# Kernel optimization log

Hardware: AMD Instinct MI355X
Metric: run time of the kernel (lower is better)

Reference implementation:

```python
import jax, jax.numpy as jnp
import numpy as np

N_NODES = 100000
N_EDGES = 2000000


def _mlp3(h, w1, b1, w2, b2, w3, b3):
    h = jax.nn.relu(h @ w1.T + b1)
    h = jax.nn.relu(h @ w2.T + b2)
    return h @ w3.T + b3


def setup_inputs() -> dict:
    key = jax.random.key(0)
    ks = jax.random.split(key, 24)
    inp = {
        "x": jax.random.normal(ks[0], (N_NODES, 3), dtype=jnp.float32),
        "edge_index": jax.random.randint(ks[1], (2, N_EDGES), 0, N_NODES, dtype=jnp.int64),
        "edge_attr": jax.random.normal(ks[2], (N_EDGES, 4), dtype=jnp.float32),
    }
    # MLP params (PyTorch Linear: y = x @ W.T + b)
    shapes = {
        "r1_w1": (40, 10), "r1_b1": (40,), "r1_w2": (40, 40), "r1_b2": (40,), "r1_w3": (4, 40), "r1_b3": (4,),
        "o_w1": (40, 7), "o_b1": (40,), "o_w2": (40, 40), "o_b2": (40,), "o_w3": (3, 40), "o_b3": (3,),
        "r2_w1": (40, 10), "r2_b1": (40,), "r2_w2": (40, 40), "r2_b2": (40,), "r2_w3": (1, 40), "r2_b3": (1,),
    }
    for i, (name, shp) in enumerate(shapes.items()):
        inp[name] = jax.random.normal(ks[3 + i], shp, dtype=jnp.float32) * 0.1
    return inp


def reference(x, edge_index, edge_attr,
              r1_w1, r1_b1, r1_w2, r1_b2, r1_w3, r1_b3,
              o_w1, o_b1, o_w2, o_b2, o_w3, o_b3,
              r2_w1, r2_b1, r2_w2, r2_b2, r2_w3, r2_b3):
    n = x.shape[0]
    src, dst = edge_index[0], edge_index[1]  # x_j <- src, x_i <- dst
    # message: relational MLP R1 over [x_i, x_j, edge_attr]  -> [E,4]
    m1 = jnp.concatenate([x[dst], x[src], edge_attr], axis=1)
    e_msg = _mlp3(m1, r1_w1, r1_b1, r1_w2, r1_b2, r1_w3, r1_b3)
    # aggregate: scatter-add messages to destination nodes -> [N,4]
    aggr = jax.ops.segment_sum(e_msg, dst, num_segments=n)
    # update: object MLP O over [x, aggr] -> [N,3]
    x_tilde = _mlp3(jnp.concatenate([x, aggr], axis=1), o_w1, o_b1, o_w2, o_b2, o_w3, o_b3)
    # edge classifier R2 over [x_tilde_i, x_tilde_j, E] -> sigmoid [E,1]
    m2 = jnp.concatenate([x_tilde[dst], x_tilde[src], e_msg], axis=1)
    return jax.nn.sigmoid(_mlp3(m2, r2_w1, r2_b1, r2_w2, r2_b2, r2_w3, r2_b3))
```

## Files before the change

kernel.cpp:

```cpp
#include <hip/hip_runtime.h>
#include <math.h>


typedef __fp16 hf8 __attribute__((ext_vector_type(8)));
typedef _Float16 f16x2 __attribute__((ext_vector_type(2)));
typedef float f32x16 __attribute__((ext_vector_type(16)));
typedef unsigned u32x4 __attribute__((ext_vector_type(4)));

#define NEPC  64
#define BS    4096
#define NBMAX 32
#define TS    1024
#define NFRAG 11

__device__ __forceinline__ f32x16 mfma16(hf8 a, hf8 b, f32x16 c) {
    return __builtin_amdgcn_mfma_f32_32x32x16_f16(a, b, c, 0, 0, 0);
}
__device__ __forceinline__ unsigned pk2(float a, float b) {
    return __builtin_bit_cast(unsigned, __builtin_amdgcn_cvt_pkrtz(a, b));
}
__device__ __forceinline__ unsigned pk2_relu(float a, float b) {
    return __builtin_bit_cast(unsigned,
        __builtin_amdgcn_cvt_pkrtz(fmaxf(a, 0.f), fmaxf(b, 0.f)));
}
__device__ __forceinline__ unsigned pswap(unsigned v) {
    return (unsigned)__shfl_xor((int)v, 32, 64);
}
__device__ __forceinline__ hf8 frag_from(unsigned a, unsigned b, unsigned c, unsigned d) {
    u32x4 v = {a, b, c, d};
    return __builtin_bit_cast(hf8, v);
}

__device__ __forceinline__ void build_frags(const f32x16& t0, const f32x16& t1,
                                            int hi, hf8& F0, hf8& F1, hf8& F2) {
    const unsigned w0 = pk2_relu(t0[0],  t0[1]);
    const unsigned w1 = pk2_relu(t0[2],  t0[3]);
    const unsigned w2 = pk2_relu(t0[4],  t0[5]);
    const unsigned w3 = pk2_relu(t0[6],  t0[7]);
    const unsigned w4 = pk2_relu(t0[8],  t0[9]);
    const unsigned w5 = pk2_relu(t0[10], t0[11]);
    const unsigned w6 = pk2_relu(t0[12], t0[13]);
    const unsigned w7 = pk2_relu(t0[14], t0[15]);
    const unsigned w8 = pk2_relu(t1[0],  t1[1]);
    const unsigned w9 = pk2_relu(t1[2],  t1[3]);
    const unsigned p0 = pswap(w0), p1 = pswap(w1), p2 = pswap(w2), p3 = pswap(w3);
    const unsigned p4 = pswap(w4), p5 = pswap(w5), p6 = pswap(w6), p7 = pswap(w7);
    const unsigned p8 = pswap(w8), p9 = pswap(w9);
    F0 = frag_from(hi ? p2 : w0, hi ? p3 : w1, hi ? w2 : p0, hi ? w3 : p1);
    F1 = frag_from(hi ? p6 : w4, hi ? p7 : w5, hi ? w6 : p4, hi ? w7 : p5);
    F2 = frag_from(hi ? 0x00003c00u : w8, hi ? 0u : w9, hi ? 0u : p8, hi ? 0u : p9);
}

template<int IN, int OUT>
__device__ hf8 load_wfrag(const float* __restrict__ w, const float* __restrict__ b,
                          int mt, int ks, int lane) {
    const int r = mt * 32 + (lane & 31);
    const int kbase = ks * 16 + ((lane >> 5) & 1) * 8;
    hf8 f;
#pragma unroll
    for (int j = 0; j < 8; ++j) {
        const int k = kbase + j;
        float v = 0.f;
        if (r < OUT) {
            if (k < IN) v = w[r * IN + k];
            else if (k == IN) v = b[r];
        }
        f[j] = (__fp16)v;
    }
    return f;
}

template<int OUT>
__device__ hf8 load_wfrag_l1(const float* __restrict__ w, const float* __restrict__ b,
                             int mt, int lane) {
    const int r = mt * 32 + (lane & 31);
    const int kbase = ((lane >> 5) & 1) * 8;
    hf8 f;
#pragma unroll
    for (int j = 0; j < 8; ++j) {
        const int k = kbase + j;
        float v = 0.f;
        if (r < OUT) {
            int src = -1;
            if (k < 3) src = k;
            else if (k >= 4 && k < 7) src = k - 1;
            else if (k >= 8 && k < 12) src = k - 2;
            if (src >= 0) v = w[r * 10 + src];
            else if (k == 12) v = b[r];
        }
        f[j] = (__fp16)v;
    }
    return f;
}

template<int OUT3>
__global__ __launch_bounds__(64) void wprep_kernel(
    const float* __restrict__ w1, const float* __restrict__ b1,
    const float* __restrict__ w2, const float* __restrict__ b2,
    const float* __restrict__ w3, const float* __restrict__ b3,
    uint4* __restrict__ tab)
{
    const int lane = threadIdx.x;
#pragma unroll
    for (int t = 0; t < 2; ++t)
        tab[t * 64 + lane] = __builtin_bit_cast(uint4, load_wfrag_l1<40>(w1, b1, t, lane));
#pragma unroll
    for (int t = 0; t < 2; ++t)
#pragma unroll
        for (int s = 0; s < 3; ++s)
            tab[(2 + t * 3 + s) * 64 + lane] =
                __builtin_bit_cast(uint4, load_wfrag<40, 40>(w2, b2, t, s, lane));
#pragma unroll
    for (int s = 0; s < 3; ++s)
        tab[(8 + s) * 64 + lane] =
            __builtin_bit_cast(uint4, load_wfrag<40, OUT3>(w3, b3, 0, s, lane));
}

template<bool IS_MSG>
__global__ __launch_bounds__(256, 2) void edge_kernel(
    const uint2* __restrict__ nodef,
    const int*   __restrict__ ei,
    const void*  __restrict__ eattr,
    const uint4* __restrict__ wtab,
    uint2* __restrict__ emsg_out,
    float* __restrict__ out,
    int n_edges)
{
    const int lane = threadIdx.x & 63;
    const int ecol = lane & 31;
    const int hi = lane >> 5;

    hf8 wa1[2], wa2[2][3], wa3[3];
    wa1[0] = __builtin_bit_cast(hf8, wtab[0 * 64 + lane]);
    wa1[1] = __builtin_bit_cast(hf8, wtab[1 * 64 + lane]);
#pragma unroll
    for (int t = 0; t < 2; ++t)
#pragma unroll
        for (int s = 0; s < 3; ++s)
            wa2[t][s] = __builtin_bit_cast(hf8, wtab[(2 + t * 3 + s) * 64 + lane]);
#pragma unroll
    for (int s = 0; s < 3; ++s)
        wa3[s] = __builtin_bit_cast(hf8, wtab[(8 + s) * 64 + lane]);

    const int gwave = (int)((blockIdx.x * blockDim.x + threadIdx.x) >> 6);
    const int nwave = (int)((gridDim.x * blockDim.x) >> 6);
    const int nchunk = (n_edges + NEPC - 1) / NEPC;
    const int last = n_edges - 1;

    int c = gwave;
    if (c >= nchunk) return;
    auto eclampX = [&](int cc) { int e = cc * NEPC + ecol;      return e < last ? e : last; };
    auto eclampY = [&](int cc) { int e = cc * NEPC + 32 + ecol; return e < last ? e : last; };

    uint2 fAX, fBX, fAY, fBY;
    int sNX = 0, dNX = 0, sNY = 0, dNY = 0;
    {
        const int eX = eclampX(c), eY = eclampY(c);
        if (hi == 0) {
            const int sX = ei[eX], dX = ei[n_edges + eX];
            const int sY = ei[eY], dY = ei[n_edges + eY];
            fAX = nodef[dX]; fBX = nodef[sX];
            fAY = nodef[dY]; fBY = nodef[sY];
            const int e2X = eclampX(c + nwave), e2Y = eclampY(c + nwave);
            sNX = ei[e2X]; dNX = ei[n_edges + e2X];
            sNY = ei[e2Y]; dNY = ei[n_edges + e2Y];
        } else {
            if (IS_MSG) {
                const float4 evX = ((const float4*)eattr)[eX];
                fAX = make_uint2(pk2(evX.x, evX.y), pk2(evX.z, evX.w));
                const float4 evY = ((const float4*)eattr)[eY];
                fAY = make_uint2(pk2(evY.x, evY.y), pk2(evY.z, evY.w));
            } else {
                fAX = ((const uint2*)eattr)[eX];
                fAY = ((const uint2*)eattr)[eY];
            }
            fBX = make_uint2(0x00003c00u, 0u);
            fBY = fBX;
        }
    }

    for (; c < nchunk; ) {
        const int cn = c + nwave;

        const hf8 bfX = frag_from(fAX.x, fAX.y, fBX.x, fBX.y);
        const hf8 bfY = frag_from(fAY.x, fAY.y, fBY.x, fBY.y);

        uint2 nfAX = fAX, nfBX = fBX, nfAY = fAY, nfBY = fBY;
        int sPX = sNX, dPX = dNX, sPY = sNY, dPY = dNY;
        {
            if (hi == 0) {
                nfAX = nodef[dNX]; nfBX = nodef[sNX];
                nfAY = nodef[dNY]; nfBY = nodef[sNY];
                const int e3X = eclampX(cn + nwave), e3Y = eclampY(cn + nwave);
                sPX = ei[e3X]; dPX = ei[n_edges + e3X];
                sPY = ei[e3Y]; dPY = ei[n_edges + e3Y];
            } else {
                const int e2X = eclampX(cn), e2Y = eclampY(cn);
                if (IS_MSG) {
                    const float4 evX = ((const float4*)eattr)[e2X];
                    nfAX = make_uint2(pk2(evX.x, evX.y), pk2(evX.z, evX.w));
                    const float4 evY = ((const float4*)eattr)[e2Y];
                    nfAY = make_uint2(pk2(evY.x, evY.y), pk2(evY.z, evY.w));
                } else {
                    nfAX = ((const uint2*)eattr)[e2X];
                    nfAY = ((const uint2*)eattr)[e2Y];
                }
            }
        }

        f32x16 a0X = {}, a1X = {}, a0Y = {}, a1Y = {};
        a0X = mfma16(wa1[0], bfX, a0X);
        a0Y = mfma16(wa1[0], bfY, a0Y);
        a1X = mfma16(wa1[1], bfX, a1X);
        a1Y = mfma16(wa1[1], bfY, a1Y);

        hf8 f0X, f1X, f2X, f0Y, f1Y, f2Y;
        build_frags(a0X, a1X, hi, f0X, f1X, f2X);
        build_frags(a0Y, a1Y, hi, f0Y, f1Y, f2Y);

        f32x16 c0X = {}, c1X = {}, c0Y = {}, c1Y = {};
        c0X = mfma16(wa2[0][0], f0X, c0X); c0Y = mfma16(wa2[0][0], f0Y, c0Y);
        c1X = mfma16(wa2[1][0], f0X, c1X); c1Y = mfma16(wa2[1][0], f0Y, c1Y);
        c0X = mfma16(wa2[0][1], f1X, c0X); c0Y = mfma16(wa2[0][1], f1Y, c0Y);
        c1X = mfma16(wa2[1][1], f1X, c1X); c1Y = mfma16(wa2[1][1], f1Y, c1Y);
        c0X = mfma16(wa2[0][2], f2X, c0X); c0Y = mfma16(wa2[0][2], f2Y, c0Y);
        c1X = mfma16(wa2[1][2], f2X, c1X); c1Y = mfma16(wa2[1][2], f2Y, c1Y);

        hf8 g0X, g1X, g2X, g0Y, g1Y, g2Y;
        build_frags(c0X, c1X, hi, g0X, g1X, g2X);
        build_frags(c0Y, c1Y, hi, g0Y, g1Y, g2Y);

        f32x16 z0X = {}, z0Y = {};
        z0X = mfma16(wa3[0], g0X, z0X); z0Y = mfma16(wa3[0], g0Y, z0Y);
        z0X = mfma16(wa3[1], g1X, z0X); z0Y = mfma16(wa3[1], g1Y, z0Y);
        z0X = mfma16(wa3[2], g2X, z0X); z0Y = mfma16(wa3[2], g2Y, z0Y);

        if (hi == 0) {
            const int eX = c * NEPC + ecol;
            const int eY = eX + 32;
            if (eX < n_edges) {
                if (IS_MSG)
                    emsg_out[eX] = make_uint2(pk2(z0X[0], z0X[1]), pk2(z0X[2], z0X[3]));
                else
                    out[eX] = 1.f / (1.f + expf(-z0X[0]));
            }
            if (eY < n_edges) {
                if (IS_MSG)
                    emsg_out[eY] = make_uint2(pk2(z0Y[0], z0Y[1]), pk2(z0Y[2], z0Y[3]));
                else
                    out[eY] = 1.f / (1.f + expf(-z0Y[0]));
            }
        }

        fAX = nfAX; fBX = nfBX; fAY = nfAY; fBY = nfBY;
        sNX = sPX; dNX = dPX; sNY = sPY; dNY = dPY;
        c = cn;
    }
}

__global__ __launch_bounds__(256) void nodef_kernel(
    const float* __restrict__ x, uint2* __restrict__ nodef, int n_nodes)
{
    int n = blockIdx.x * blockDim.x + threadIdx.x;
    if (n >= n_nodes) return;
    nodef[n] = make_uint2(pk2(x[n * 3 + 0], x[n * 3 + 1]), pk2(x[n * 3 + 2], 0.f));
}

__global__ __launch_bounds__(TS) void count_kernel(
    const int* __restrict__ dstp, unsigned* __restrict__ tilecnt, int n_edges)
{
    __shared__ unsigned lc[NBMAX];
    const int tid = threadIdx.x;
    if (tid < NBMAX) lc[tid] = 0u;
    __syncthreads();
    const int e = blockIdx.x * TS + tid;
    if (e < n_edges) atomicAdd(&lc[((unsigned)dstp[e]) >> 12], 1u);
    __syncthreads();
    if (tid < NBMAX) tilecnt[(size_t)blockIdx.x * NBMAX + tid] = lc[tid];
}

__global__ __launch_bounds__(1024) void scan_kernel(
    unsigned* __restrict__ tilecnt, unsigned* __restrict__ totals, int ntiles)
{
    __shared__ unsigned buf[1024];
    const int b = blockIdx.x;
    const int tid = threadIdx.x;
    unsigned carry = 0;
    for (int base = 0; base < ntiles; base += 1024) {
        const int i = base + tid;
        const unsigned v = (i < ntiles) ? tilecnt[(size_t)i * NBMAX + b] : 0u;
        buf[tid] = v;
        __syncthreads();
        for (int off = 1; off < 1024; off <<= 1) {
            const unsigned t = (tid >= off) ? buf[tid - off] : 0u;
            __syncthreads();
            buf[tid] += t;
            __syncthreads();
        }
        if (i < ntiles) tilecnt[(size_t)i * NBMAX + b] = (buf[tid] - v) + carry;
        carry += buf[1023];
        __syncthreads();
    }
    if (tid == 0) totals[b] = carry;
}

__global__ __launch_bounds__(64) void base_kernel(
    const unsigned* __restrict__ totals, unsigned* __restrict__ bases, int nbins)
{
    if (threadIdx.x == 0) {
        unsigned run = 0;
        for (int i = 0; i < nbins; ++i) { bases[i] = run; run += totals[i]; }
    }
}

__global__ __launch_bounds__(TS) void split_kernel(
    const int* __restrict__ dstp,
    const uint2* __restrict__ emsg,
    const unsigned* __restrict__ tilecnt,
    const unsigned* __restrict__ bases,
    unsigned* __restrict__ bd,
    uint2* __restrict__ bm,
    int n_edges, int nbins)
{
    __shared__ unsigned lcnt[NBMAX], loff[NBMAX], gbase[NBMAX];
    __shared__ unsigned stage[TS * 3];
    const int tid = threadIdx.x;
    const int e = blockIdx.x * TS + tid;
    const bool valid = e < n_edges;

    if (tid < NBMAX) lcnt[tid] = 0u;
    __syncthreads();

    unsigned d = 0, b = 0, slot = 0; uint2 m = make_uint2(0u, 0u);
    if (valid) {
        d = (unsigned)dstp[e];
        m = emsg[e];
        b = d >> 12;
        slot = atomicAdd(&lcnt[b], 1u);
    }
    __syncthreads();

    if (tid < NBMAX && tid < (unsigned)nbins) {
        gbase[tid] = bases[tid] + tilecnt[(size_t)blockIdx.x * NBMAX + tid];
    }
    if (tid == 0) {
        unsigned run = 0;
        for (int i = 0; i < nbins; ++i) { loff[i] = run; run += lcnt[i]; }
    }
    __syncthreads();

    if (valid) {
        const unsigned p = (loff[b] + slot) * 3;
        stage[p] = d; stage[p + 1] = m.x; stage[p + 2] = m.y;
    }
    __syncthreads();

    const int total = min(TS, n_edges - blockIdx.x * TS);
    if (tid < total) {
        const unsigned dd = stage[tid * 3];
        const unsigned bb = dd >> 12;
        const unsigned gpos = gbase[bb] + ((unsigned)tid - loff[bb]);
        bd[gpos] = dd;
        bm[gpos] = make_uint2(stage[tid * 3 + 1], stage[tid * 3 + 2]);
    }
}

typedef _Float16 hf2 __attribute__((ext_vector_type(2)));
__global__ __launch_bounds__(1024) void accum_kernel(
    const unsigned* __restrict__ bd,
    const uint2* __restrict__ bm,
    const unsigned* __restrict__ totals,
    const unsigned* __restrict__ bases,
    uint2* __restrict__ scratch,
    int S)
{
    __shared__ unsigned bin[BS * 2];
    const int bid = blockIdx.x / S, s = blockIdx.x % S;
    const int tid = threadIdx.x;

#pragma unroll
    for (int i = 0; i < (BS * 2) / 1024; ++i)
        bin[tid + i * 1024] = 0u;
    __syncthreads();

    const unsigned start = bases[bid], len = totals[bid];
    const unsigned r0 = start + (unsigned)((unsigned long long)len * s / S);
    const unsigned r1 = start + (unsigned)((unsigned long long)len * (s + 1) / S);
    for (unsigned r = r0 + tid; r < r1; r += 1024) {
        const unsigned d = bd[r];
        const uint2 m = bm[r];
        const unsigned laddr =
            (unsigned)(reinterpret_cast<uintptr_t>(&bin[(d & (BS - 1)) * 2]));
        asm volatile("ds_pk_add_f16 %0, %1" :: "v"(laddr), "v"(m.x) : "memory");
        asm volatile("ds_pk_add_f16 %0, %1 offset:4" :: "v"(laddr), "v"(m.y) : "memory");
    }
    __syncthreads();

    uint2* dst = scratch + (size_t)(bid * S + s) * BS;
    const uint2* srcb = (const uint2*)bin;
#pragma unroll
    for (int i = 0; i < BS / 1024; ++i)
        dst[tid + i * 1024] = srcb[tid + i * 1024];
}

__global__ __launch_bounds__(256) void reduce_kernel(
    const uint2* __restrict__ scratch,
    float* __restrict__ aggr,
    int n_nodes, int S)
{
    int n = blockIdx.x * blockDim.x + threadIdx.x;
    if (n >= n_nodes) return;
    const int b = n / BS, nl = n % BS;
    float4 acc = make_float4(0.f, 0.f, 0.f, 0.f);
    for (int w = 0; w < S; ++w) {
        const uint2 v = scratch[(size_t)(b * S + w) * BS + nl];
        const hf2 lo = __builtin_bit_cast(hf2, v.x);
        const hf2 hi = __builtin_bit_cast(hf2, v.y);
        acc.x += (float)lo.x; acc.y += (float)lo.y;
        acc.z += (float)hi.x; acc.w += (float)hi.y;
    }
    *(float4*)(aggr + (size_t)n * 4) = acc;
}

template<int IN, int OUT, bool RELU>
__device__ __forceinline__ void dense(const float* __restrict__ w,
                                      const float* __restrict__ b,
                                      const float* in, float* out) {
#pragma unroll
    for (int j = 0; j < OUT; ++j) {
        float acc = b[j];
#pragma unroll
        for (int k = 0; k < IN; ++k) acc = fmaf(w[j * IN + k], in[k], acc);
        out[j] = RELU ? fmaxf(acc, 0.f) : acc;
    }
}

__global__ __launch_bounds__(256) void node_kernel(
    const float* __restrict__ x,
    const float* __restrict__ aggr,
    const float* __restrict__ w1, const float* __restrict__ b1,
    const float* __restrict__ w2, const float* __restrict__ b2,
    const float* __restrict__ w3, const float* __restrict__ b3,
    uint2* __restrict__ xth,
    int n_nodes)
{
    int n = blockIdx.x * blockDim.x + threadIdx.x;
    if (n >= n_nodes) return;

    float in[7];
    in[0] = x[n * 3 + 0]; in[1] = x[n * 3 + 1]; in[2] = x[n * 3 + 2];
    const float4 ag = *(const float4*)(aggr + (size_t)n * 4);
    in[3] = ag.x; in[4] = ag.y; in[5] = ag.z; in[6] = ag.w;

    float h1[40], h2[40], o[3];
    dense<7, 40, true >(w1, b1, in, h1);
    dense<40, 40, true>(w2, b2, h1, h2);
    dense<40, 3, false>(w3, b3, h2, o);

    xth[n] = make_uint2(pk2(o[0], o[1]), pk2(o[2], 0.f));
}

extern "C" void kernel_launch(void* const* d_in, const int* in_sizes, int n_in,
                              void* d_out, int out_size, void* d_ws, size_t ws_size,
                              hipStream_t stream) {
    const float* x  = (const float*)d_in[0];
    const int*   ei = (const int*)d_in[1];
    const float* ea = (const float*)d_in[2];

    const float* r1_w1 = (const float*)d_in[3];
    const float* r1_b1 = (const float*)d_in[4];
    const float* r1_w2 = (const float*)d_in[5];
    const float* r1_b2 = (const float*)d_in[6];
    const float* r1_w3 = (const float*)d_in[7];
    const float* r1_b3 = (const float*)d_in[8];

    const float* o_w1 = (const float*)d_in[9];
    const float* o_b1 = (const float*)d_in[10];
    const float* o_w2 = (const float*)d_in[11];
    const float* o_b2 = (const float*)d_in[12];
    const float* o_w3 = (const float*)d_in[13];
    const float* o_b3 = (const float*)d_in[14];

    const float* r2_w1 = (const float*)d_in[15];
    const float* r2_b1 = (const float*)d_in[16];
    const float* r2_w2 = (const float*)d_in[17];
    const float* r2_b2 = (const float*)d_in[18];
    const float* r2_w3 = (const float*)d_in[19];
    const float* r2_b3 = (const float*)d_in[20];

    const int n_nodes = in_sizes[0] / 3;
    const int n_edges = in_sizes[2] / 4;
    const int B = (n_nodes + BS - 1) / BS;
    const int ntiles = (n_edges + TS - 1) / TS;

    uint2*    nodef   = (uint2*)d_ws;
    float*    aggr    = (float*)(nodef + n_nodes);
    uint2*    emsg    = (uint2*)(aggr + (size_t)n_nodes * 4);
    unsigned* bd      = (unsigned*)(emsg + n_edges);
    uint2*    bm      = (uint2*)(bd + n_edges);
    unsigned* totals  = (unsigned*)(bm + n_edges);
    unsigned* bases   = totals + NBMAX;
    unsigned* tilecnt = bases + NBMAX;
    uint4*    wtab1   = (uint4*)(tilecnt + (size_t)ntiles * NBMAX);
    uint4*    wtab2   = wtab1 + NFRAG * 64;
    uint2*    scratch = (uint2*)(wtab2 + NFRAG * 64);

    const size_t fixed_bytes = (char*)scratch - (char*)d_ws;
    int S = 16;
    while (S > 4 && ws_size < fixed_bytes + (size_t)B * S * BS * sizeof(uint2))
        S >>= 1;

    const int eb = 1024;
    const int nb = (n_nodes + 255) / 256;

    wprep_kernel<4><<<1, 64, 0, stream>>>(r1_w1, r1_b1, r1_w2, r1_b2,
                                          r1_w3, r1_b3, wtab1);
    wprep_kernel<1><<<1, 64, 0, stream>>>(r2_w1, r2_b1, r2_w2, r2_b2,
                                          r2_w3, r2_b3, wtab2);

    nodef_kernel<<<nb, 256, 0, stream>>>(x, nodef, n_nodes);

    edge_kernel<true><<<eb, 256, 0, stream>>>(nodef, ei, (const void*)ea,
        wtab1, emsg, nullptr, n_edges);

    count_kernel<<<ntiles, TS, 0, stream>>>(ei + n_edges, tilecnt, n_edges);

    scan_kernel<<<B, 1024, 0, stream>>>(tilecnt, totals, ntiles);

    base_kernel<<<1, 64, 0, stream>>>(totals, bases, B);

    split_kernel<<<ntiles, TS, 0, stream>>>(ei + n_edges, emsg, tilecnt, bases,
                                            bd, bm, n_edges, B);

    accum_kernel<<<B * S, 1024, 0, stream>>>(bd, bm, totals, bases, scratch, S);

    reduce_kernel<<<nb, 256, 0, stream>>>(scratch, aggr, n_nodes, S);

    node_kernel<<<nb, 256, 0, stream>>>(x, aggr,
        o_w1, o_b1, o_w2, o_b2, o_w3, o_b3, nodef, n_nodes);

    edge_kernel<false><<<eb, 256, 0, stream>>>(nodef, ei, (const void*)emsg,
        wtab2, nullptr, (float*)d_out, n_edges);
}
```

Before: 181.9 us.

## Merge weight-prep launches, raise edge kernel occupancy, unroll accumulation loads

Combines the two weight-preparation kernels into one two-block launch, with the block index choosing which MLP's weights to process, to save a kernel launch. Raises the edge kernel's launch-bounds occupancy hint from 2 to 3 blocks per SM, which may force the compiler to use fewer registers and spill. Unrolls the accum_kernel loop 4x so that global loads are issued ahead of the LDS packed atomics, improving memory-level parallelism.

```diff
diff --git a/kernel.cpp b/kernel.cpp
--- a/kernel.cpp
+++ b/kernel.cpp
@@ -51,9 +51,8 @@
     F2 = frag_from(hi ? 0x00003c00u : w8, hi ? 0u : w9, hi ? 0u : p8, hi ? 0u : p9);
 }
 
-template<int IN, int OUT>
-__device__ hf8 load_wfrag(const float* __restrict__ w, const float* __restrict__ b,
-                          int mt, int ks, int lane) {
+__device__ hf8 load_wfrag40(const float* __restrict__ w, const float* __restrict__ b,
+                            int OUT, int mt, int ks, int lane) {
     const int r = mt * 32 + (lane & 31);
     const int kbase = ks * 16 + ((lane >> 5) & 1) * 8;
     hf8 f;
@@ -62,15 +61,14 @@
         const int k = kbase + j;
         float v = 0.f;
         if (r < OUT) {
-            if (k < IN) v = w[r * IN + k];
-            else if (k == IN) v = b[r];
+            if (k < 40) v = w[r * 40 + k];
+            else if (k == 40) v = b[r];
         }
         f[j] = (__fp16)v;
     }
     return f;
 }
 
-template<int OUT>
 __device__ hf8 load_wfrag_l1(const float* __restrict__ w, const float* __restrict__ b,
                              int mt, int lane) {
     const int r = mt * 32 + (lane & 31);
@@ -80,7 +78,7 @@
     for (int j = 0; j < 8; ++j) {
         const int k = kbase + j;
         float v = 0.f;
-        if (r < OUT) {
+        if (r < 40) {
             int src = -1;
             if (k < 3) src = k;
             else if (k >= 4 && k < 7) src = k - 1;
@@ -93,31 +91,39 @@
     return f;
 }
 
-template<int OUT3>
 __global__ __launch_bounds__(64) void wprep_kernel(
-    const float* __restrict__ w1, const float* __restrict__ b1,
-    const float* __restrict__ w2, const float* __restrict__ b2,
-    const float* __restrict__ w3, const float* __restrict__ b3,
-    uint4* __restrict__ tab)
+    const float* __restrict__ a_w1, const float* __restrict__ a_b1,
+    const float* __restrict__ a_w2, const float* __restrict__ a_b2,
+    const float* __restrict__ a_w3, const float* __restrict__ a_b3,
+    const float* __restrict__ b_w1, const float* __restrict__ b_b1,
+    const float* __restrict__ b_w2, const float* __restrict__ b_b2,
+    const float* __restrict__ b_w3, const float* __restrict__ b_b3,
+    uint4* __restrict__ tab1, uint4* __restrict__ tab2)
 {
     const int lane = threadIdx.x;
+    const bool second = blockIdx.x == 1;
+    const float* w1 = second ? b_w1 : a_w1; const float* b1 = second ? b_b1 : a_b1;
+    const float* w2 = second ? b_w2 : a_w2; const float* b2 = second ? b_b2 : a_b2;
+    const float* w3 = second ? b_w3 : a_w3; const float* b3 = second ? b_b3 : a_b3;
+    uint4* tab = second ? tab2 : tab1;
+    const int out3 = second ? 1 : 4;
 #pragma unroll
     for (int t = 0; t < 2; ++t)
-        tab[t * 64 + lane] = __builtin_bit_cast(uint4, load_wfrag_l1<40>(w1, b1, t, lane));
+        tab[t * 64 + lane] = __builtin_bit_cast(uint4, load_wfrag_l1(w1, b1, t, lane));
 #pragma unroll
     for (int t = 0; t < 2; ++t)
 #pragma unroll
         for (int s = 0; s < 3; ++s)
             tab[(2 + t * 3 + s) * 64 + lane] =
-                __builtin_bit_cast(uint4, load_wfrag<40, 40>(w2, b2, t, s, lane));
+                __builtin_bit_cast(uint4, load_wfrag40(w2, b2, 40, t, s, lane));
 #pragma unroll
     for (int s = 0; s < 3; ++s)
         tab[(8 + s) * 64 + lane] =
-            __builtin_bit_cast(uint4, load_wfrag<40, OUT3>(w3, b3, 0, s, lane));
+            __builtin_bit_cast(uint4, load_wfrag40(w3, b3, out3, 0, s, lane));
 }
 
 template<bool IS_MSG>
-__global__ __launch_bounds__(256, 2) void edge_kernel(
+__global__ __launch_bounds__(256, 3) void edge_kernel(
     const uint2* __restrict__ nodef,
     const int*   __restrict__ ei,
     const void*  __restrict__ eattr,
@@ -366,6 +372,14 @@
 }
 
 typedef _Float16 hf2 __attribute__((ext_vector_type(2)));
+__device__ __forceinline__ void pk_accum(unsigned* __restrict__ bin,
+                                         unsigned d, uint2 m) {
+    const unsigned laddr =
+        (unsigned)(reinterpret_cast<uintptr_t>(&bin[(d & (BS - 1)) * 2]));
+    asm volatile("ds_pk_add_f16 %0, %1" :: "v"(laddr), "v"(m.x) : "memory");
+    asm volatile("ds_pk_add_f16 %0, %1 offset:4" :: "v"(laddr), "v"(m.y) : "memory");
+}
+
 __global__ __launch_bounds__(1024) void accum_kernel(
     const unsigned* __restrict__ bd,
     const uint2* __restrict__ bm,
@@ -386,14 +400,18 @@
     const unsigned start = bases[bid], len = totals[bid];
     const unsigned r0 = start + (unsigned)((unsigned long long)len * s / S);
     const unsigned r1 = start + (unsigned)((unsigned long long)len * (s + 1) / S);
-    for (unsigned r = r0 + tid; r < r1; r += 1024) {
-        const unsigned d = bd[r];
-        const uint2 m = bm[r];
-        const unsigned laddr =
-            (unsigned)(reinterpret_cast<uintptr_t>(&bin[(d & (BS - 1)) * 2]));
-        asm volatile("ds_pk_add_f16 %0, %1" :: "v"(laddr), "v"(m.x) : "memory");
-        asm volatile("ds_pk_add_f16 %0, %1 offset:4" :: "v"(laddr), "v"(m.y) : "memory");
-    }
+
+    unsigned r = r0 + tid;
+    for (; r + 3072 < r1; r += 4096) {
+        const unsigned d0 = bd[r], d1 = bd[r + 1024], d2 = bd[r + 2048], d3 = bd[r + 3072];
+        const uint2 m0 = bm[r], m1 = bm[r + 1024], m2 = bm[r + 2048], m3 = bm[r + 3072];
+        pk_accum(bin, d0, m0);
+        pk_accum(bin, d1, m1);
+        pk_accum(bin, d2, m2);
+        pk_accum(bin, d3, m3);
+    }
+    for (; r < r1; r += 1024)
+        pk_accum(bin, bd[r], bm[r]);
     __syncthreads();
 
     uint2* dst = scratch + (size_t)(bid * S + s) * BS;
@@ -513,10 +531,9 @@
     const int eb = 1024;
     const int nb = (n_nodes + 255) / 256;
 
-    wprep_kernel<4><<<1, 64, 0, stream>>>(r1_w1, r1_b1, r1_w2, r1_b2,
-                                          r1_w3, r1_b3, wtab1);
-    wprep_kernel<1><<<1, 64, 0, stream>>>(r2_w1, r2_b1, r2_w2, r2_b2,
-                                          r2_w3, r2_b3, wtab2);
+    wprep_kernel<<<2, 64, 0, stream>>>(r1_w1, r1_b1, r1_w2, r1_b2, r1_w3, r1_b3,
+                                       r2_w1, r2_b1, r2_w2, r2_b2, r2_w3, r2_b3,
+                                       wtab1, wtab2);
 
     nodef_kernel<<<nb, 256, 0, stream>>>(x, nodef, n_nodes);
 
```

After: 176.5 us. 1.03x faster.
